# Kernel tuning notes

Measured on AMD Instinct MI355X. Metric: run time of the kernel, lower is better.

Reference implementation:

```python
import jax, jax.numpy as jnp
import numpy as np

B, C, L = 16, 256, 2048


def setup_inputs() -> dict:
    key = jax.random.key(0)
    ks = jax.random.split(key, 7)
    s = 0.05
    return {
        "x": jax.random.normal(ks[0], (B, C, L), dtype=jnp.float32),
        "W_theta": jax.random.normal(ks[1], (C, C), dtype=jnp.float32) * s,
        "b_theta": jax.random.normal(ks[2], (C,), dtype=jnp.float32) * s,
        "W_phi": jax.random.normal(ks[3], (C, C), dtype=jnp.float32) * s,
        "b_phi": jax.random.normal(ks[4], (C,), dtype=jnp.float32) * s,
        "W_g": jax.random.normal(ks[5], (C, C), dtype=jnp.float32) * s,
        "b_g": jax.random.normal(ks[6], (C,), dtype=jnp.float32) * s,
    }


def reference(x, W_theta, b_theta, W_phi, b_phi, W_g, b_g):
    # x: [B, C, L]; 1x1 Conv1d == linear over channel dim: out[b,o,l] = W[o,c] x[b,c,l] + b[o]
    q = jnp.einsum('oc,bcl->bol', W_theta, x) + b_theta[None, :, None]  # [B,C,L]
    k = jnp.einsum('oc,bcl->bol', W_phi, x) + b_phi[None, :, None]
    v = jnp.einsum('oc,bcl->bol', W_g, x) + b_g[None, :, None]
    num_c = x.shape[1]
    # scores[b,i,j] = sum_c q[b,c,i] * k[b,c,j]
    scores = jnp.einsum('bci,bcj->bij', q, k) / jnp.sqrt(jnp.float32(num_c))  # [B,L,L]
    attn = jax.nn.softmax(scores, axis=-1)
    # out[b,i,c] = sum_j attn[b,i,j] v[b,c,j]; then permute back to [B,C,L]
    attn_out = jnp.einsum('bij,bcj->bci', attn, v)  # [B,C,L]
    return x + attn_out
```

## Files before the change

### kernel.cpp

```cpp
#include <hip/hip_runtime.h>
#include <math.h>

#define B_ 16
#define C_ 256
#define L_ 2048

using short8 = __attribute__((ext_vector_type(8))) short;
using f32x4  = __attribute__((ext_vector_type(4))) float;

__device__ __forceinline__ unsigned short f2bf(float f) {
  unsigned u = __float_as_uint(f);
  return (unsigned short)((u + 0x7FFFu + ((u >> 16) & 1u)) >> 16);
}

__device__ __forceinline__ void gload16(const void* src, void* dst) {
  __builtin_amdgcn_global_load_lds(
      (const __attribute__((address_space(1))) unsigned int*)src,
      (__attribute__((address_space(3))) unsigned int*)dst, 16, 0, 0);
}

__global__ __launch_bounds__(256) void convert_w(const float* __restrict__ wt,
                                                 const float* __restrict__ wp,
                                                 const float* __restrict__ wg,
                                                 unsigned short* __restrict__ dst) {
  int i = blockIdx.x * 256 + threadIdx.x;
  dst[i]          = f2bf(wt[i]);
  dst[65536 + i]  = f2bf(wp[i]);
  dst[131072 + i] = f2bf(wg[i]);
}

__global__ __launch_bounds__(256, 2) void proj_kernel(
    const float* __restrict__ x, const unsigned short* __restrict__ wbf,
    const float* __restrict__ bth, const float* __restrict__ bph,
    const float* __restrict__ bg,
    unsigned short* __restrict__ qT, unsigned short* __restrict__ kT,
    unsigned short* __restrict__ vv)
{
  const int tid  = threadIdx.x;
  const int w    = tid >> 6;
  const int lane = tid & 63;
  const int r    = lane & 15;
  const int g    = lane >> 4;
  const int l0   = blockIdx.x * 64;
  const int b    = blockIdx.y;
  const int p    = blockIdx.z;

  __shared__ unsigned short xs[64 * 64];
  __shared__ unsigned short wsd[256 * 64];

  const unsigned short* wsrc = wbf + p * 65536;

  f32x4 acc[4][4];
#pragma unroll
  for (int mi = 0; mi < 4; ++mi)
#pragma unroll
    for (int ni = 0; ni < 4; ++ni) acc[mi][ni] = f32x4{0.f, 0.f, 0.f, 0.f};

  for (int ks = 0; ks < 4; ++ks) {
    __syncthreads();
#pragma unroll
    for (int it = 0; it < 8; ++it) {
      int d  = it * 256 + w * 64 + lane;
      int o  = d >> 3;
      int cs = d & 7;
      const unsigned short* src = wsrc + o * C_ + ks * 64 + ((cs ^ (o & 7)) << 3);
      gload16(src, (void*)(wsd + (size_t)(it * 256 + w * 64) * 8));
    }
#pragma unroll
    for (int it = 0; it < 16; ++it) {
      int l = (tid & 15) + 16 * (it & 3);
      int c = (tid >> 4) + 16 * (it >> 2);
      float xvv = x[((size_t)b * C_ + ks * 64 + c) * L_ + l0 + l];
      xs[l * 64 + (((c >> 3) ^ (l & 7)) << 3) + (c & 7)] = f2bf(xvv);
    }
    __syncthreads();

#pragma unroll
    for (int kk2 = 0; kk2 < 2; ++kk2) {
      short8 xf[4], wf[4];
#pragma unroll
      for (int i = 0; i < 4; ++i) {
        int lrow = 16 * i + r;
        xf[i] = *(const short8*)(xs + lrow * 64 + (((kk2 * 4 + g) ^ (lrow & 7)) << 3));
        int orow = 64 * w + 16 * i + r;
        wf[i] = *(const short8*)(wsd + orow * 64 + (((kk2 * 4 + g) ^ (orow & 7)) << 3));
      }
      if (p < 2) {
#pragma unroll
        for (int mi = 0; mi < 4; ++mi)
#pragma unroll
          for (int ni = 0; ni < 4; ++ni)
            acc[mi][ni] = __builtin_amdgcn_mfma_f32_16x16x32_bf16(xf[mi], wf[ni], acc[mi][ni], 0, 0, 0);
      } else {
#pragma unroll
        for (int mi = 0; mi < 4; ++mi)
#pragma unroll
          for (int ni = 0; ni < 4; ++ni)
            acc[mi][ni] = __builtin_amdgcn_mfma_f32_16x16x32_bf16(wf[mi], xf[ni], acc[mi][ni], 0, 0, 0);
      }
    }
  }

  if (p < 2) {
    unsigned short* dst = (p == 0) ? qT : kT;
    const float* bias   = (p == 0) ? bth : bph;
    const float scale   = (p == 0) ? 0.09016844005556021f : 1.0f;
#pragma unroll
    for (int ni = 0; ni < 4; ++ni) {
      int o    = 64 * w + 16 * ni + r;
      float bv = bias[o];
#pragma unroll
      for (int mi = 0; mi < 4; ++mi)
#pragma unroll
        for (int rr = 0; rr < 4; ++rr) {
          int l = l0 + 16 * mi + 4 * g + rr;
          dst[((size_t)b * L_ + l) * C_ + o] = f2bf((acc[mi][ni][rr] + bv) * scale);
        }
    }
  } else {
#pragma unroll
    for (int mi = 0; mi < 4; ++mi)
#pragma unroll
      for (int rr = 0; rr < 4; ++rr) {
        int o    = 64 * w + 16 * mi + 4 * g + rr;
        float bv = bg[o];
#pragma unroll
        for (int ni = 0; ni < 4; ++ni) {
          int l = l0 + 16 * ni + r;
          vv[((size_t)b * C_ + o) * L_ + l] = f2bf(acc[mi][ni][rr] + bv);
        }
      }
  }
}

__global__ __launch_bounds__(256, 2) void attn_kernel(
    const unsigned short* __restrict__ qT, const unsigned short* __restrict__ kT,
    const unsigned short* __restrict__ vv,
    const float* __restrict__ x, float* __restrict__ out)
{
  const int tid  = threadIdx.x;
  const int w    = tid >> 6;
  const int lane = tid & 63;
  const int r    = lane & 15;
  const int g    = lane >> 4;

  int wg = ((blockIdx.x & 7) << 6) | (blockIdx.x >> 3);
  const int i0 = (wg & 31) * 64;
  const int b  = wg >> 5;

  __shared__ unsigned short kls[64 * 256];
  __shared__ unsigned short vls[256 * 64];
  __shared__ unsigned short pls[64 * 64];
  __shared__ float lsums[64];

  short8 qf[8];
  const int qrow = i0 + 16 * w + r;
#pragma unroll
  for (int kk = 0; kk < 8; ++kk)
    qf[kk] = *(const short8*)(qT + ((size_t)b * L_ + qrow) * C_ + kk * 32 + 8 * g);

  f32x4 oacc[4][4];
#pragma unroll
  for (int mi = 0; mi < 4; ++mi)
#pragma unroll
    for (int nf = 0; nf < 4; ++nf) oacc[mi][nf] = f32x4{0.f, 0.f, 0.f, 0.f};
  float lsum[4] = {0.f, 0.f, 0.f, 0.f};

  const unsigned short* kTb = kT + (size_t)b * L_ * C_;
  const unsigned short* vvb = vv + (size_t)b * C_ * L_;

  for (int jt = 0; jt < 32; ++jt) {
    const int j0 = jt * 64;
    __syncthreads();
#pragma unroll
    for (int it = 0; it < 8; ++it) {
      int d   = it * 256 + w * 64 + lane;
      int row = d >> 5;
      int cs  = d & 31;
      const unsigned short* src = kTb + (size_t)(j0 + row) * C_ + ((cs ^ (row & 7)) << 3);
      gload16(src, (void*)(kls + (size_t)(it * 256 + w * 64) * 8));
    }
#pragma unroll
    for (int it = 0; it < 8; ++it) {
      int d   = it * 256 + w * 64 + lane;
      int row = d >> 3;
      int cs  = d & 7;
      const unsigned short* src = vvb + (size_t)row * L_ + j0 + ((cs ^ (row & 7)) << 3);
      gload16(src, (void*)(vls + (size_t)(it * 256 + w * 64) * 8));
    }
    __syncthreads();

    f32x4 sacc[4];
#pragma unroll
    for (int ni = 0; ni < 4; ++ni) sacc[ni] = f32x4{0.f, 0.f, 0.f, 0.f};
#pragma unroll
    for (int kk = 0; kk < 8; ++kk) {
#pragma unroll
      for (int ni = 0; ni < 4; ++ni) {
        int jrow = 16 * ni + r;
        short8 kf = *(const short8*)(kls + jrow * 256 + (((4 * kk + g) ^ (jrow & 7)) << 3));
        sacc[ni] = __builtin_amdgcn_mfma_f32_16x16x32_bf16(qf[kk], kf, sacc[ni], 0, 0, 0);
      }
    }

#pragma unroll
    for (int ni = 0; ni < 4; ++ni) {
#pragma unroll
      for (int rr = 0; rr < 4; ++rr) {
        float pv = exp2f(sacc[ni][rr]);
        lsum[rr] += pv;
        int irow = 16 * w + 4 * g + rr;
        int j    = r + 16 * ni;
        pls[irow * 64 + (((j >> 3) ^ (irow & 7)) << 3) + (j & 7)] = f2bf(pv);
      }
    }
    __syncthreads();

#pragma unroll
    for (int kk2 = 0; kk2 < 2; ++kk2) {
      short8 pf[4];
#pragma unroll
      for (int mi = 0; mi < 4; ++mi) {
        int irow = 16 * mi + r;
        pf[mi] = *(const short8*)(pls + irow * 64 + (((4 * kk2 + g) ^ (irow & 7)) << 3));
      }
#pragma unroll
      for (int nf = 0; nf < 4; ++nf) {
        int crow = 64 * w + 16 * nf + r;
        short8 vf = *(const short8*)(vls + crow * 64 + (((4 * kk2 + g) ^ (crow & 7)) << 3));
#pragma unroll
        for (int mi = 0; mi < 4; ++mi)
          oacc[mi][nf] = __builtin_amdgcn_mfma_f32_16x16x32_bf16(pf[mi], vf, oacc[mi][nf], 0, 0, 0);
      }
    }
  }

#pragma unroll
  for (int off = 1; off < 16; off <<= 1)
#pragma unroll
    for (int rr = 0; rr < 4; ++rr) lsum[rr] += __shfl_xor(lsum[rr], off);
  if (r == 0) {
    f32x4 t{lsum[0], lsum[1], lsum[2], lsum[3]};
    *(f32x4*)(lsums + 16 * w + 4 * g) = t;
  }
  __syncthreads();

#pragma unroll
  for (int mi = 0; mi < 4; ++mi) {
    f32x4 ls = *(const f32x4*)(lsums + 16 * mi + 4 * g);
    f32x4 linv;
#pragma unroll
    for (int rr = 0; rr < 4; ++rr) linv[rr] = 1.0f / ls[rr];
#pragma unroll
    for (int nf = 0; nf < 4; ++nf) {
      int c = 64 * w + 16 * nf + r;
      size_t base = ((size_t)b * C_ + c) * L_ + i0 + 16 * mi + 4 * g;
      f32x4 xv = *(const f32x4*)(x + base);
      f32x4 ov;
#pragma unroll
      for (int rr = 0; rr < 4; ++rr) ov[rr] = xv[rr] + oacc[mi][nf][rr] * linv[rr];
      *(f32x4*)(out + base) = ov;
    }
  }
}

extern "C" void kernel_launch(void* const* d_in, const int* in_sizes, int n_in,
                              void* d_out, int out_size, void* d_ws, size_t ws_size,
                              hipStream_t stream) {
  (void)in_sizes; (void)n_in; (void)out_size; (void)ws_size;
  const float* x   = (const float*)d_in[0];
  const float* wt  = (const float*)d_in[1];
  const float* bt  = (const float*)d_in[2];
  const float* wp  = (const float*)d_in[3];
  const float* bp  = (const float*)d_in[4];
  const float* wg  = (const float*)d_in[5];
  const float* bgg = (const float*)d_in[6];
  float* out = (float*)d_out;

  char* ws = (char*)d_ws;
  unsigned short* wbf = (unsigned short*)ws;
  unsigned short* qT  = (unsigned short*)(ws + 393216);
  unsigned short* kT  = (unsigned short*)(ws + 393216 + 16777216);
  unsigned short* vv  = (unsigned short*)(ws + 393216 + 2 * 16777216);

  convert_w<<<dim3(256), dim3(256), 0, stream>>>(wt, wp, wg, wbf);
  proj_kernel<<<dim3(32, 16, 3), dim3(256), 0, stream>>>(x, wbf, bt, bp, bgg, qT, kT, vv);
  attn_kernel<<<dim3(512), dim3(256), 0, stream>>>(qT, kT, vv, x, out);
}
```

Measured before the change: 140.1 us.

## Fuse three projections per block and restructure attention loop with K prefetch and register V

The projection kernel now loads and converts the whole x tile to bf16 once and loops over all three weight matrices, replacing three blocks that each re-read x. The attention kernel drops the shared V buffer and loads V fragments straight from global memory into registers. It prefetches the next K tile into shared memory during the P·V phase and computes S transposed so each lane owns one row. It also uses inline v_exp_f32 and packed bf16 conversion, raises MFMA wave priority with s_setprio, and bumps the occupancy hint to 3 blocks per SM. The risks are uncoalesced direct V global loads, higher register pressure, and a single K buffer whose overlap relies on the barrier ordering being correct.

```diff
diff --git a/kernel.cpp b/kernel.cpp
--- a/kernel.cpp
+++ b/kernel.cpp
@@ -1,5 +1,4 @@
 #include <hip/hip_runtime.h>
-#include <math.h>
 
 #define B_ 16
 #define C_ 256
@@ -7,6 +6,7 @@
 
 using short8 = __attribute__((ext_vector_type(8))) short;
 using f32x4  = __attribute__((ext_vector_type(4))) float;
+typedef unsigned int uint;
 
 __device__ __forceinline__ unsigned short f2bf(float f) {
   unsigned u = __float_as_uint(f);
@@ -43,97 +43,98 @@
   const int g    = lane >> 4;
   const int l0   = blockIdx.x * 64;
   const int b    = blockIdx.y;
-  const int p    = blockIdx.z;
-
-  __shared__ unsigned short xs[64 * 64];
+
+  __shared__ unsigned short xs[64 * 256];
   __shared__ unsigned short wsd[256 * 64];
 
-  const unsigned short* wsrc = wbf + p * 65536;
+#pragma unroll
+  for (int it = 0; it < 64; ++it) {
+    int l = (tid & 15) + 16 * (it & 3);
+    int c = (tid >> 4) + 16 * (it >> 2);
+    float xvv = x[((size_t)b * C_ + c) * L_ + l0 + l];
+    xs[l * 256 + (((c >> 3) ^ (l & 7)) << 3) + (c & 7)] = f2bf(xvv);
+  }
 
   f32x4 acc[4][4];
-#pragma unroll
-  for (int mi = 0; mi < 4; ++mi)
-#pragma unroll
-    for (int ni = 0; ni < 4; ++ni) acc[mi][ni] = f32x4{0.f, 0.f, 0.f, 0.f};
-
-  for (int ks = 0; ks < 4; ++ks) {
-    __syncthreads();
-#pragma unroll
-    for (int it = 0; it < 8; ++it) {
-      int d  = it * 256 + w * 64 + lane;
-      int o  = d >> 3;
-      int cs = d & 7;
-      const unsigned short* src = wsrc + o * C_ + ks * 64 + ((cs ^ (o & 7)) << 3);
-      gload16(src, (void*)(wsd + (size_t)(it * 256 + w * 64) * 8));
-    }
-#pragma unroll
-    for (int it = 0; it < 16; ++it) {
-      int l = (tid & 15) + 16 * (it & 3);
-      int c = (tid >> 4) + 16 * (it >> 2);
-      float xvv = x[((size_t)b * C_ + ks * 64 + c) * L_ + l0 + l];
-      xs[l * 64 + (((c >> 3) ^ (l & 7)) << 3) + (c & 7)] = f2bf(xvv);
-    }
-    __syncthreads();
-
-#pragma unroll
-    for (int kk2 = 0; kk2 < 2; ++kk2) {
-      short8 xf[4], wf[4];
-#pragma unroll
-      for (int i = 0; i < 4; ++i) {
-        int lrow = 16 * i + r;
-        xf[i] = *(const short8*)(xs + lrow * 64 + (((kk2 * 4 + g) ^ (lrow & 7)) << 3));
-        int orow = 64 * w + 16 * i + r;
-        wf[i] = *(const short8*)(wsd + orow * 64 + (((kk2 * 4 + g) ^ (orow & 7)) << 3));
-      }
-      if (p < 2) {
+  for (int p = 0; p < 3; ++p) {
+    const unsigned short* wsrc = wbf + p * 65536;
+#pragma unroll
+    for (int mi = 0; mi < 4; ++mi)
+#pragma unroll
+      for (int ni = 0; ni < 4; ++ni) acc[mi][ni] = f32x4{0.f, 0.f, 0.f, 0.f};
+
+    for (int ks = 0; ks < 4; ++ks) {
+      __syncthreads();
+#pragma unroll
+      for (int it = 0; it < 8; ++it) {
+        int o  = it * 32 + (tid >> 3);
+        int cs = tid & 7;
+        gload16(wsrc + o * C_ + ks * 64 + ((cs ^ (o & 7)) << 3),
+                (void*)(wsd + (size_t)(it * 256 + w * 64) * 8));
+      }
+      __syncthreads();
+
+#pragma unroll
+      for (int kk2 = 0; kk2 < 2; ++kk2) {
+        short8 xf[4], wf[4];
+#pragma unroll
+        for (int i = 0; i < 4; ++i) {
+          int lrow = 16 * i + r;
+          xf[i] = *(const short8*)(xs + lrow * 256 +
+                                   (((8 * ks + 4 * kk2 + g) ^ (lrow & 7)) << 3));
+          int orow = 64 * w + 16 * i + r;
+          wf[i] = *(const short8*)(wsd + orow * 64 + (((kk2 * 4 + g) ^ (orow & 7)) << 3));
+        }
+        if (p < 2) {
+#pragma unroll
+          for (int mi = 0; mi < 4; ++mi)
+#pragma unroll
+            for (int ni = 0; ni < 4; ++ni)
+              acc[mi][ni] = __builtin_amdgcn_mfma_f32_16x16x32_bf16(xf[mi], wf[ni], acc[mi][ni], 0, 0, 0);
+        } else {
+#pragma unroll
+          for (int mi = 0; mi < 4; ++mi)
+#pragma unroll
+            for (int ni = 0; ni < 4; ++ni)
+              acc[mi][ni] = __builtin_amdgcn_mfma_f32_16x16x32_bf16(wf[mi], xf[ni], acc[mi][ni], 0, 0, 0);
+        }
+      }
+    }
+
+    if (p < 2) {
+      unsigned short* dst = (p == 0) ? qT : kT;
+      const float* bias   = (p == 0) ? bth : bph;
+      const float scale   = (p == 0) ? 0.09016844005556021f : 1.0f;
+#pragma unroll
+      for (int ni = 0; ni < 4; ++ni) {
+        int o    = 64 * w + 16 * ni + r;
+        float bv = bias[o];
 #pragma unroll
         for (int mi = 0; mi < 4; ++mi)
 #pragma unroll
-          for (int ni = 0; ni < 4; ++ni)
-            acc[mi][ni] = __builtin_amdgcn_mfma_f32_16x16x32_bf16(xf[mi], wf[ni], acc[mi][ni], 0, 0, 0);
-      } else {
-#pragma unroll
-        for (int mi = 0; mi < 4; ++mi)
-#pragma unroll
-          for (int ni = 0; ni < 4; ++ni)
-            acc[mi][ni] = __builtin_amdgcn_mfma_f32_16x16x32_bf16(wf[mi], xf[ni], acc[mi][ni], 0, 0, 0);
-      }
-    }
-  }
-
-  if (p < 2) {
-    unsigned short* dst = (p == 0) ? qT : kT;
-    const float* bias   = (p == 0) ? bth : bph;
-    const float scale   = (p == 0) ? 0.09016844005556021f : 1.0f;
-#pragma unroll
-    for (int ni = 0; ni < 4; ++ni) {
-      int o    = 64 * w + 16 * ni + r;
-      float bv = bias[o];
+          for (int rr = 0; rr < 4; ++rr) {
+            int l = l0 + 16 * mi + 4 * g + rr;
+            dst[((size_t)b * L_ + l) * C_ + o] = f2bf((acc[mi][ni][rr] + bv) * scale);
+          }
+      }
+    } else {
 #pragma unroll
       for (int mi = 0; mi < 4; ++mi)
 #pragma unroll
         for (int rr = 0; rr < 4; ++rr) {
-          int l = l0 + 16 * mi + 4 * g + rr;
-          dst[((size_t)b * L_ + l) * C_ + o] = f2bf((acc[mi][ni][rr] + bv) * scale);
+          int o    = 64 * w + 16 * mi + 4 * g + rr;
+          float bv = bg[o];
+#pragma unroll
+          for (int ni = 0; ni < 4; ++ni) {
+            int l = l0 + 16 * ni + r;
+            vv[((size_t)b * C_ + o) * L_ + l] = f2bf(acc[mi][ni][rr] + bv);
+          }
         }
     }
-  } else {
-#pragma unroll
-    for (int mi = 0; mi < 4; ++mi)
-#pragma unroll
-      for (int rr = 0; rr < 4; ++rr) {
-        int o    = 64 * w + 16 * mi + 4 * g + rr;
-        float bv = bg[o];
-#pragma unroll
-        for (int ni = 0; ni < 4; ++ni) {
-          int l = l0 + 16 * ni + r;
-          vv[((size_t)b * C_ + o) * L_ + l] = f2bf(acc[mi][ni][rr] + bv);
-        }
-      }
-  }
-}
-
-__global__ __launch_bounds__(256, 2) void attn_kernel(
+  }
+}
+
+__global__ __launch_bounds__(256, 3) void attn_kernel(
     const unsigned short* __restrict__ qT, const unsigned short* __restrict__ kT,
     const unsigned short* __restrict__ vv,
     const float* __restrict__ x, float* __restrict__ out)
@@ -149,100 +150,108 @@
   const int b  = wg >> 5;
 
   __shared__ unsigned short kls[64 * 256];
-  __shared__ unsigned short vls[256 * 64];
   __shared__ unsigned short pls[64 * 64];
   __shared__ float lsums[64];
 
-  short8 qf[8];
-  const int qrow = i0 + 16 * w + r;
-#pragma unroll
-  for (int kk = 0; kk < 8; ++kk)
-    qf[kk] = *(const short8*)(qT + ((size_t)b * L_ + qrow) * C_ + kk * 32 + 8 * g);
-
-  f32x4 oacc[4][4];
-#pragma unroll
-  for (int mi = 0; mi < 4; ++mi)
-#pragma unroll
-    for (int nf = 0; nf < 4; ++nf) oacc[mi][nf] = f32x4{0.f, 0.f, 0.f, 0.f};
-  float lsum[4] = {0.f, 0.f, 0.f, 0.f};
-
   const unsigned short* kTb = kT + (size_t)b * L_ * C_;
   const unsigned short* vvb = vv + (size_t)b * C_ * L_;
+
+  short8 qf[8];
+  const unsigned short* qrow_p = qT + ((size_t)b * L_ + i0 + 16 * w + r) * C_;
+#pragma unroll
+  for (int kk = 0; kk < 8; ++kk)
+    qf[kk] = *(const short8*)(qrow_p + kk * 32 + 8 * g);
+
+  f32x4 oacc[4][4];
+#pragma unroll
+  for (int mi = 0; mi < 4; ++mi)
+#pragma unroll
+    for (int nf = 0; nf < 4; ++nf) oacc[mi][nf] = f32x4{0.f, 0.f, 0.f, 0.f};
+  float lsum = 0.f;
+
+#pragma unroll
+  for (int it = 0; it < 8; ++it) {
+    int d   = it * 256 + tid;
+    int row = d >> 5;
+    int cs  = d & 31;
+    gload16(kTb + (size_t)row * C_ + ((cs ^ (row & 7)) << 3), (void*)(kls + d * 8));
+  }
 
   for (int jt = 0; jt < 32; ++jt) {
     const int j0 = jt * 64;
     __syncthreads();
-#pragma unroll
-    for (int it = 0; it < 8; ++it) {
-      int d   = it * 256 + w * 64 + lane;
-      int row = d >> 5;
-      int cs  = d & 31;
-      const unsigned short* src = kTb + (size_t)(j0 + row) * C_ + ((cs ^ (row & 7)) << 3);
-      gload16(src, (void*)(kls + (size_t)(it * 256 + w * 64) * 8));
-    }
-#pragma unroll
-    for (int it = 0; it < 8; ++it) {
-      int d   = it * 256 + w * 64 + lane;
-      int row = d >> 3;
-      int cs  = d & 7;
-      const unsigned short* src = vvb + (size_t)row * L_ + j0 + ((cs ^ (row & 7)) << 3);
-      gload16(src, (void*)(vls + (size_t)(it * 256 + w * 64) * 8));
+
+    short8 vfr[2][4];
+#pragma unroll
+    for (int kk2 = 0; kk2 < 2; ++kk2)
+#pragma unroll
+      for (int nf = 0; nf < 4; ++nf)
+        vfr[kk2][nf] = *(const short8*)(vvb + (size_t)(64 * w + 16 * nf + r) * L_ +
+                                        j0 + 32 * kk2 + 8 * g);
+
+    f32x4 sacc[4];
+#pragma unroll
+    for (int ni = 0; ni < 4; ++ni) sacc[ni] = f32x4{0.f, 0.f, 0.f, 0.f};
+    __builtin_amdgcn_s_setprio(1);
+#pragma unroll
+    for (int kk = 0; kk < 8; ++kk) {
+#pragma unroll
+      for (int ni = 0; ni < 4; ++ni) {
+        int jr = 16 * ni + r;
+        short8 kf = *(const short8*)(kls + jr * 256 + (((4 * kk + g) ^ (r & 7)) << 3));
+        sacc[ni] = __builtin_amdgcn_mfma_f32_16x16x32_bf16(kf, qf[kk], sacc[ni], 0, 0, 0);
+      }
+    }
+    __builtin_amdgcn_s_setprio(0);
+
+#pragma unroll
+    for (int ni = 0; ni < 4; ++ni) {
+      float p0, p1, p2, p3;
+      asm("v_exp_f32 %0, %1" : "=v"(p0) : "v"(sacc[ni][0]));
+      asm("v_exp_f32 %0, %1" : "=v"(p1) : "v"(sacc[ni][1]));
+      asm("v_exp_f32 %0, %1" : "=v"(p2) : "v"(sacc[ni][2]));
+      asm("v_exp_f32 %0, %1" : "=v"(p3) : "v"(sacc[ni][3]));
+      lsum += (p0 + p1) + (p2 + p3);
+      uint dlo, dhi;
+      asm("v_cvt_pk_bf16_f32 %0, %1, %2" : "=v"(dlo) : "v"(p0), "v"(p1));
+      asm("v_cvt_pk_bf16_f32 %0, %1, %2" : "=v"(dhi) : "v"(p2), "v"(p3));
+      uint2 d2; d2.x = dlo; d2.y = dhi;
+      *(uint2*)(pls + (16 * w + r) * 64 + (((4 * ni + g) ^ ((r & 7) << 1)) << 2)) = d2;
     }
     __syncthreads();
 
-    f32x4 sacc[4];
-#pragma unroll
-    for (int ni = 0; ni < 4; ++ni) sacc[ni] = f32x4{0.f, 0.f, 0.f, 0.f};
-#pragma unroll
-    for (int kk = 0; kk < 8; ++kk) {
-#pragma unroll
-      for (int ni = 0; ni < 4; ++ni) {
-        int jrow = 16 * ni + r;
-        short8 kf = *(const short8*)(kls + jrow * 256 + (((4 * kk + g) ^ (jrow & 7)) << 3));
-        sacc[ni] = __builtin_amdgcn_mfma_f32_16x16x32_bf16(qf[kk], kf, sacc[ni], 0, 0, 0);
-      }
-    }
-
-#pragma unroll
-    for (int ni = 0; ni < 4; ++ni) {
-#pragma unroll
-      for (int rr = 0; rr < 4; ++rr) {
-        float pv = exp2f(sacc[ni][rr]);
-        lsum[rr] += pv;
-        int irow = 16 * w + 4 * g + rr;
-        int j    = r + 16 * ni;
-        pls[irow * 64 + (((j >> 3) ^ (irow & 7)) << 3) + (j & 7)] = f2bf(pv);
-      }
-    }
-    __syncthreads();
-
+    if (jt < 31) {
+#pragma unroll
+      for (int it = 0; it < 8; ++it) {
+        int d   = it * 256 + tid;
+        int row = d >> 5;
+        int cs  = d & 31;
+        gload16(kTb + (size_t)(j0 + 64 + row) * C_ + ((cs ^ (row & 7)) << 3),
+                (void*)(kls + d * 8));
+      }
+    }
+
+    __builtin_amdgcn_s_setprio(1);
 #pragma unroll
     for (int kk2 = 0; kk2 < 2; ++kk2) {
       short8 pf[4];
 #pragma unroll
       for (int mi = 0; mi < 4; ++mi) {
         int irow = 16 * mi + r;
-        pf[mi] = *(const short8*)(pls + irow * 64 + (((4 * kk2 + g) ^ (irow & 7)) << 3));
-      }
-#pragma unroll
-      for (int nf = 0; nf < 4; ++nf) {
-        int crow = 64 * w + 16 * nf + r;
-        short8 vf = *(const short8*)(vls + crow * 64 + (((4 * kk2 + g) ^ (crow & 7)) << 3));
+        pf[mi] = *(const short8*)(pls + irow * 64 + (((4 * kk2 + g) ^ (r & 7)) << 3));
+      }
+#pragma unroll
+      for (int nf = 0; nf < 4; ++nf)
 #pragma unroll
         for (int mi = 0; mi < 4; ++mi)
-          oacc[mi][nf] = __builtin_amdgcn_mfma_f32_16x16x32_bf16(pf[mi], vf, oacc[mi][nf], 0, 0, 0);
-      }
-    }
-  }
-
-#pragma unroll
-  for (int off = 1; off < 16; off <<= 1)
-#pragma unroll
-    for (int rr = 0; rr < 4; ++rr) lsum[rr] += __shfl_xor(lsum[rr], off);
-  if (r == 0) {
-    f32x4 t{lsum[0], lsum[1], lsum[2], lsum[3]};
-    *(f32x4*)(lsums + 16 * w + 4 * g) = t;
-  }
+          oacc[mi][nf] = __builtin_amdgcn_mfma_f32_16x16x32_bf16(pf[mi], vfr[kk2][nf], oacc[mi][nf], 0, 0, 0);
+    }
+    __builtin_amdgcn_s_setprio(0);
+  }
+
+  lsum += __shfl_xor(lsum, 16);
+  lsum += __shfl_xor(lsum, 32);
+  if (lane < 16) lsums[16 * w + lane] = lsum;
   __syncthreads();
 
 #pragma unroll
@@ -258,7 +267,8 @@
       f32x4 xv = *(const f32x4*)(x + base);
       f32x4 ov;
 #pragma unroll
-      for (int rr = 0; rr < 4; ++rr) ov[rr] = xv[rr] + oacc[mi][nf][rr] * linv[rr];
+      for (int rr = 0; rr < 4; ++rr)
+        ov[rr] = xv[rr] + oacc[mi][nf][rr] * linv[rr];
       *(f32x4*)(out + base) = ov;
     }
   }
@@ -284,6 +294,6 @@
   unsigned short* vv  = (unsigned short*)(ws + 393216 + 2 * 16777216);
 
   convert_w<<<dim3(256), dim3(256), 0, stream>>>(wt, wp, wg, wbf);
-  proj_kernel<<<dim3(32, 16, 3), dim3(256), 0, stream>>>(x, wbf, bt, bp, bgg, qT, kT, vv);
+  proj_kernel<<<dim3(32, 16), dim3(256), 0, stream>>>(x, wbf, bt, bp, bgg, qT, kT, vv);
   attn_kernel<<<dim3(512), dim3(256), 0, stream>>>(qT, kT, vv, x, out);
 }
```

Result: slower. 189.1 us (+35.0%).
